# Kernel optimization log

Hardware: AMD Instinct MI355X
Metric: run time of the kernel (lower is better)

Reference implementation:

```python
import jax, jax.numpy as jnp
import numpy as np

B, N = 32, 256
PHI1, PHI2 = 64, 128
RHO1, RHO2, OUT = 256, 128, 64


def setup_inputs() -> dict:
    key = jax.random.key(0)
    ks = jax.random.split(key, 12)
    dm = jax.random.normal(ks[0], (B, N, N), dtype=jnp.float32)
    lengths = jnp.clip(jax.random.randint(ks[1], (B,), 0, N), 2, N).astype(jnp.int32)

    def lin(k, fan_in, fan_out):
        # torch nn.Linear default init: U(-1/sqrt(fan_in), 1/sqrt(fan_in))
        bound = 1.0 / np.sqrt(fan_in)
        kw, kb = jax.random.split(k)
        W = jax.random.uniform(kw, (fan_in, fan_out), jnp.float32, -bound, bound)
        b = jax.random.uniform(kb, (fan_out,), jnp.float32, -bound, bound)
        return W, b

    W1, b1 = lin(ks[2], 1, PHI1)
    W2, b2 = lin(ks[3], PHI1, PHI2)
    W3, b3 = lin(ks[4], PHI2, RHO1)
    W4, b4 = lin(ks[5], RHO1, RHO2)
    W5, b5 = lin(ks[6], RHO2, OUT)
    return {"dm": dm, "lengths": lengths, "W1": W1, "b1": b1, "W2": W2, "b2": b2,
            "W3": W3, "b3": b3, "W4": W4, "b4": b4, "W5": W5, "b5": b5}


def reference(dm, lengths, W1, b1, W2, b2, W3, b3, W4, b4, W5, b5):
    # Static upper-triangular (offset=1) index pairs: P = N*(N-1)/2
    iu0, iu1 = jnp.triu_indices(N, k=1)
    scalars = dm[:, iu0, iu1]                                   # [B, P]
    # Ragged mask: a pair (i, j) exists only if both indices < item length
    mask = (iu0[None, :] < lengths[:, None]) & (iu1[None, :] < lengths[:, None])  # [B, P]
    # phi MLP applied per scalar: 1 -> 64 -> 128, ReLU after each
    h = jax.nn.relu(scalars[..., None] * W1[0] + b1)            # [B, P, 64]
    h = jax.nn.relu(jnp.einsum('bpd,de->bpe', h, W2) + b2)      # [B, P, 128]
    # Masked sum-pool over pairs
    pooled = jnp.sum(h * mask[..., None].astype(h.dtype), axis=1)  # [B, 128]
    # rho MLP: 128 -> 256 -> 128 -> OUT (ReLU on hidden layers only)
    r = jax.nn.relu(pooled @ W3 + b3)
    r = jax.nn.relu(r @ W4 + b4)
    return r @ W5 + b5                                           # [B, OUT]
```

## Files before the change

kernel.cpp:

```cpp
#include <hip/hip_runtime.h>
#include <hip/hip_bf16.h>


#define NB 32
#define NN 256
#define PHI2 128
#define SEGS 65

__global__ __launch_bounds__(128) void build_tables(
    const float* __restrict__ W1, const float* __restrict__ b1,
    const float* __restrict__ W2, const float* __restrict__ b2,
    float4* __restrict__ table4,
    float* __restrict__ tsort, float* __restrict__ pooled) {
  __shared__ float w2_s[64 * PHI2];
  __shared__ float t_s[64], w1_s[64], b1_s[64];
  __shared__ float a_sh[128], b_sh[128];
  __shared__ int cat_s[64], rank_s[64];
  const int tid = threadIdx.x;
  const int seg = blockIdx.x;
  const float4* W2v = (const float4*)W2;
  float4* w2v = (float4*)w2_s;
  for (int i = tid; i < 64 * PHI2 / 4; i += 128) w2v[i] = W2v[i];
  if (tid < 64) {
    float w = W1[tid], bb = b1[tid];
    w1_s[tid] = w; b1_s[tid] = bb;
    int cat; float t;
    if (w > 0.f)      { cat = 0; t = -bb / w; }
    else if (w < 0.f) { cat = 1; t = -bb / w; }
    else              { cat = (bb > 0.f) ? 2 : 3; t = 0.f; }
    t_s[tid] = t; cat_s[tid] = cat;
  }
  __syncthreads();
  if (tid < 64) {
    float t = t_s[tid]; int r = 0;
    for (int k = 0; k < 64; ++k) {
      float tk = t_s[k];
      r += (tk < t) || (tk == t && k < tid);
    }
    rank_s[tid] = r;
    if (seg == 0) tsort[r] = t;
  }
  __syncthreads();
  float a = 0.f, bsum = b2[tid];
#pragma unroll 8
  for (int j = 0; j < 64; ++j) {
    int cat = cat_s[j], r = rank_s[j];
    bool act = (cat == 0) ? (seg > r) : (cat == 1) ? (seg <= r) : (cat == 2);
    float w2 = w2_s[j * PHI2 + tid];
    float m = act ? 1.f : 0.f;
    a    = fmaf(m * w1_s[j], w2, a);
    bsum = fmaf(m * b1_s[j], w2, bsum);
  }
  a_sh[tid] = a; b_sh[tid] = bsum;
  __syncthreads();
  if (tid < 64)
    table4[seg * 64 + tid] =
        make_float4(a_sh[tid], b_sh[tid], a_sh[tid + 64], b_sh[tid + 64]);
  if (seg == 0) {
    for (int i = tid; i < NB * PHI2; i += 128) pooled[i] = 0.f;
  }
}

__device__ __forceinline__ void visit(float comp, int L, float tv, int lane,
                                      const float4* ab_s, float& acc0,
                                      float& acc1) {
  float s = __int_as_float(__builtin_amdgcn_readlane(__float_as_int(comp), L));
  int pos = (int)__popcll(__ballot(tv < s));
  float4 p = ab_s[pos * 64 + lane];
  acc0 += fmaxf(fmaf(p.x, s, p.y), 0.f);
  acc1 += fmaxf(fmaf(p.z, s, p.w), 0.f);
}

__device__ __forceinline__ void visit_dyn(const float4& f4, int j, float tv,
                                          int lane, const float4* ab_s,
                                          float& acc0, float& acc1) {
  int c = j & 3;
  float comp = (c == 0) ? f4.x : (c == 1) ? f4.y : (c == 2) ? f4.z : f4.w;
  visit(comp, j >> 2, tv, lane, ab_s, acc0, acc1);
}

__device__ __forceinline__ void do_row(const float4& f4, int i0, int len,
                                       int half, float tv, int lane,
                                       const float4* ab_s, float& acc0,
                                       float& acc1) {
  const int jlo = i0 + 1, jhi = len - 1;
  const int fullLo = (jlo + 3) >> 2;
  const int fullHi = (jhi >= 3) ? ((jhi - 3) >> 2) : -1;
  if (fullLo > fullHi) {
    for (int j = jlo; j <= jhi; ++j)
      if (((j >> 2) & 1) == half) visit_dyn(f4, j, tv, lane, ab_s, acc0, acc1);
    return;
  }
  for (int j = jlo; j < fullLo * 4; ++j)
    if (((j >> 2) & 1) == half) visit_dyn(f4, j, tv, lane, ab_s, acc0, acc1);
  int L0 = fullLo + (((fullLo & 1) != half) ? 1 : 0);
#pragma unroll 2
  for (int L = L0; L <= fullHi; L += 2) {
    visit(f4.x, L, tv, lane, ab_s, acc0, acc1);
    visit(f4.y, L, tv, lane, ab_s, acc0, acc1);
    visit(f4.z, L, tv, lane, ab_s, acc0, acc1);
    visit(f4.w, L, tv, lane, ab_s, acc0, acc1);
  }
  for (int j = fullHi * 4 + 4; j <= jhi; ++j)
    if (((j >> 2) & 1) == half) visit_dyn(f4, j, tv, lane, ab_s, acc0, acc1);
}

__global__ __launch_bounds__(1024, 8) void phi_pool(
    const float* __restrict__ dm, const int* __restrict__ lengths,
    const float4* __restrict__ table4, const float* __restrict__ tsort,
    float* __restrict__ pooled) {
  __shared__ float4 ab_s[SEGS * 64];
  const int c_row = blockIdx.x >> 1;
  const int half  = blockIdx.x & 1;
  const int b     = blockIdx.y;
  const int tid = threadIdx.x;
  const int lane = tid & 63, w = tid >> 6;

  const int len = lengths[b];
  if (c_row * 16 > len - 2 && 239 - c_row * 16 > len - 2) return;

  for (int i = tid; i < SEGS * 64; i += 1024) ab_s[i] = table4[i];
  __syncthreads();

  const float tv = tsort[lane];
  const float* dmb = dm + (size_t)b * (NN * NN);
  float acc0 = 0.f, acc1 = 0.f;

  const int rA = c_row * 16 + w;
  const int rB = 254 - rA;
  const float4 fA = ((const float4*)(dmb + rA * NN))[lane];
  const float4 fB = ((const float4*)(dmb + rB * NN))[lane];
  if (rA <= len - 2) do_row(fA, rA, len, half, tv, lane, ab_s, acc0, acc1);
  if (rB != rA && rB <= len - 2)
    do_row(fB, rB, len, half, tv, lane, ab_s, acc0, acc1);

  atomicAdd(&pooled[b * PHI2 + lane], acc0);
  atomicAdd(&pooled[b * PHI2 + 64 + lane], acc1);
}

__global__ __launch_bounds__(256) void rho_mlp(
    const float* __restrict__ pooled,
    const float* __restrict__ W3, const float* __restrict__ b3,
    const float* __restrict__ W4, const float* __restrict__ b4,
    const float* __restrict__ W5, const float* __restrict__ b5,
    float* __restrict__ out) {
  __shared__ float w_s[128 * 256];
  __shared__ float p_s[128], r1_s[256], r2_s[128];
  const int b = blockIdx.x, tid = threadIdx.x;
  float4* wsv = (float4*)w_s;
  {
    const float4* w3v = (const float4*)W3;
    for (int i = tid; i < 8192; i += 256) wsv[i] = w3v[i];
  }
  if (tid < 128) p_s[tid] = pooled[b * 128 + tid];
  __syncthreads();
  {
    float acc = b3[tid];
#pragma unroll 8
    for (int k = 0; k < 128; ++k) acc = fmaf(p_s[k], w_s[k * 256 + tid], acc);
    r1_s[tid] = fmaxf(acc, 0.f);
  }
  __syncthreads();
  {
    const float4* w4v = (const float4*)W4;
    for (int i = tid; i < 8192; i += 256) wsv[i] = w4v[i];
  }
  __syncthreads();
  if (tid < 128) {
    float acc = b4[tid];
#pragma unroll 8
    for (int k = 0; k < 256; ++k) acc = fmaf(r1_s[k], w_s[k * 128 + tid], acc);
    r2_s[tid] = fmaxf(acc, 0.f);
  }
  __syncthreads();
  {
    const float4* w5v = (const float4*)W5;
    for (int i = tid; i < 2048; i += 256) wsv[i] = w5v[i];
  }
  __syncthreads();
  if (tid < 64) {
    float acc = b5[tid];
#pragma unroll 8
    for (int k = 0; k < 128; ++k) acc = fmaf(r2_s[k], w_s[k * 64 + tid], acc);
    out[b * 64 + tid] = acc;
  }
}

extern "C" void kernel_launch(void* const* d_in, const int* in_sizes, int n_in,
                              void* d_out, int out_size, void* d_ws, size_t ws_size,
                              hipStream_t stream) {
  const float* dm      = (const float*)d_in[0];
  const int*   lengths = (const int*)d_in[1];
  const float* W1 = (const float*)d_in[2];
  const float* b1 = (const float*)d_in[3];
  const float* W2 = (const float*)d_in[4];
  const float* b2 = (const float*)d_in[5];
  const float* W3 = (const float*)d_in[6];
  const float* b3 = (const float*)d_in[7];
  const float* W4 = (const float*)d_in[8];
  const float* b4 = (const float*)d_in[9];
  const float* W5 = (const float*)d_in[10];
  const float* b5 = (const float*)d_in[11];

  float* ws = (float*)d_ws;
  float4* table4 = (float4*)ws;
  float* tsort   = ws + 16640;
  float* pooled  = ws + 16704;

  build_tables<<<SEGS, 128, 0, stream>>>(W1, b1, W2, b2, table4, tsort, pooled);
  phi_pool<<<dim3(16, NB), 1024, 0, stream>>>(dm, lengths, table4, tsort, pooled);
  rho_mlp<<<NB, 256, 0, stream>>>(pooled, W3, b3, W4, b4, W5, b5, (float*)d_out);
}
```

Baseline: 133.3 us.

## Fuse rho MLP into phi pooling kernel via last-block atomic counter

```diff
diff --git a/kernel.cpp b/kernel.cpp
--- a/kernel.cpp
+++ b/kernel.cpp
@@ -11,7 +11,8 @@
     const float* __restrict__ W1, const float* __restrict__ b1,
     const float* __restrict__ W2, const float* __restrict__ b2,
     float4* __restrict__ table4,
-    float* __restrict__ tsort, float* __restrict__ pooled) {
+    float* __restrict__ tsort, float* __restrict__ pooled,
+    int* __restrict__ ctr) {
   __shared__ float w2_s[64 * PHI2];
   __shared__ float t_s[64], w1_s[64], b1_s[64];
   __shared__ float a_sh[128], b_sh[128];
@@ -58,6 +59,7 @@
         make_float4(a_sh[tid], b_sh[tid], a_sh[tid + 64], b_sh[tid + 64]);
   if (seg == 0) {
     for (int i = tid; i < NB * PHI2; i += 128) pooled[i] = 0.f;
+    if (tid < NB) ctr[tid] = 0;
   }
 }
 
@@ -105,11 +107,17 @@
     if (((j >> 2) & 1) == half) visit_dyn(f4, j, tv, lane, ab_s, acc0, acc1);
 }
 
-__global__ __launch_bounds__(1024, 8) void phi_pool(
+__global__ __launch_bounds__(1024, 8) void phi_pool_rho(
     const float* __restrict__ dm, const int* __restrict__ lengths,
     const float4* __restrict__ table4, const float* __restrict__ tsort,
-    float* __restrict__ pooled) {
+    float* __restrict__ pooled, int* __restrict__ ctr,
+    const float* __restrict__ W3, const float* __restrict__ b3,
+    const float* __restrict__ W4, const float* __restrict__ b4,
+    const float* __restrict__ W5, const float* __restrict__ b5,
+    float* __restrict__ out) {
   __shared__ float4 ab_s[SEGS * 64];
+  __shared__ float p_s[128], r1_s[256], r2_s[128];
+  __shared__ int lastflag;
   const int c_row = blockIdx.x >> 1;
   const int half  = blockIdx.x & 1;
   const int b     = blockIdx.y;
@@ -117,72 +125,90 @@
   const int lane = tid & 63, w = tid >> 6;
 
   const int len = lengths[b];
-  if (c_row * 16 > len - 2 && 239 - c_row * 16 > len - 2) return;
-
-  for (int i = tid; i < SEGS * 64; i += 1024) ab_s[i] = table4[i];
-  __syncthreads();
-
-  const float tv = tsort[lane];
-  const float* dmb = dm + (size_t)b * (NN * NN);
-  float acc0 = 0.f, acc1 = 0.f;
-
-  const int rA = c_row * 16 + w;
-  const int rB = 254 - rA;
-  const float4 fA = ((const float4*)(dmb + rA * NN))[lane];
-  const float4 fB = ((const float4*)(dmb + rB * NN))[lane];
-  if (rA <= len - 2) do_row(fA, rA, len, half, tv, lane, ab_s, acc0, acc1);
-  if (rB != rA && rB <= len - 2)
-    do_row(fB, rB, len, half, tv, lane, ab_s, acc0, acc1);
-
-  atomicAdd(&pooled[b * PHI2 + lane], acc0);
-  atomicAdd(&pooled[b * PHI2 + 64 + lane], acc1);
-}
-
-__global__ __launch_bounds__(256) void rho_mlp(
-    const float* __restrict__ pooled,
-    const float* __restrict__ W3, const float* __restrict__ b3,
-    const float* __restrict__ W4, const float* __restrict__ b4,
-    const float* __restrict__ W5, const float* __restrict__ b5,
-    float* __restrict__ out) {
-  __shared__ float w_s[128 * 256];
-  __shared__ float p_s[128], r1_s[256], r2_s[128];
-  const int b = blockIdx.x, tid = threadIdx.x;
-  float4* wsv = (float4*)w_s;
+  const bool work = !(c_row * 16 > len - 2 && 239 - c_row * 16 > len - 2);
+
+  if (work) {
+    for (int i = tid; i < SEGS * 64; i += 1024) ab_s[i] = table4[i];
+    __syncthreads();
+
+    const float tv = tsort[lane];
+    const float* dmb = dm + (size_t)b * (NN * NN);
+    float acc0 = 0.f, acc1 = 0.f;
+
+    const int rA = c_row * 16 + w;
+    const int rB = 254 - rA;
+    const float4 fA = ((const float4*)(dmb + rA * NN))[lane];
+    const float4 fB = ((const float4*)(dmb + rB * NN))[lane];
+    if (rA <= len - 2) do_row(fA, rA, len, half, tv, lane, ab_s, acc0, acc1);
+    if (rB != rA && rB <= len - 2)
+      do_row(fB, rB, len, half, tv, lane, ab_s, acc0, acc1);
+
+    atomicAdd(&pooled[b * PHI2 + lane], acc0);
+    atomicAdd(&pooled[b * PHI2 + 64 + lane], acc1);
+  }
+
+  __threadfence();
+  if (tid == 0) lastflag = (atomicAdd(&ctr[b], 1) == 15);
+  __syncthreads();
+  if (!lastflag) return;
+
+  if (tid < 128) p_s[tid] = atomicAdd(&pooled[b * PHI2 + tid], 0.0f);
+
+  float* wbuf = (float*)ab_s;
+  float4* wbv = (float4*)wbuf;
+
+  float acc = (tid < 256) ? b3[tid] : 0.f;
   {
     const float4* w3v = (const float4*)W3;
-    for (int i = tid; i < 8192; i += 256) wsv[i] = w3v[i];
-  }
-  if (tid < 128) p_s[tid] = pooled[b * 128 + tid];
-  __syncthreads();
-  {
-    float acc = b3[tid];
-#pragma unroll 8
-    for (int k = 0; k < 128; ++k) acc = fmaf(p_s[k], w_s[k * 256 + tid], acc);
-    r1_s[tid] = fmaxf(acc, 0.f);
-  }
-  __syncthreads();
+    __syncthreads();
+    for (int i = tid; i < 4096; i += 1024) wbv[i] = w3v[i];
+    __syncthreads();
+    if (tid < 256) {
+#pragma unroll 8
+      for (int k = 0; k < 64; ++k) acc = fmaf(p_s[k], wbuf[k * 256 + tid], acc);
+    }
+    __syncthreads();
+    for (int i = tid; i < 4096; i += 1024) wbv[i] = w3v[4096 + i];
+    __syncthreads();
+    if (tid < 256) {
+#pragma unroll 8
+      for (int k = 0; k < 64; ++k)
+        acc = fmaf(p_s[64 + k], wbuf[k * 256 + tid], acc);
+      r1_s[tid] = fmaxf(acc, 0.f);
+    }
+  }
   {
     const float4* w4v = (const float4*)W4;
-    for (int i = tid; i < 8192; i += 256) wsv[i] = w4v[i];
-  }
-  __syncthreads();
-  if (tid < 128) {
-    float acc = b4[tid];
-#pragma unroll 8
-    for (int k = 0; k < 256; ++k) acc = fmaf(r1_s[k], w_s[k * 128 + tid], acc);
-    r2_s[tid] = fmaxf(acc, 0.f);
-  }
-  __syncthreads();
+    __syncthreads();
+    for (int i = tid; i < 4096; i += 1024) wbv[i] = w4v[i];
+    __syncthreads();
+    float a2 = (tid < 128) ? b4[tid] : 0.f;
+    if (tid < 128) {
+#pragma unroll 8
+      for (int k = 0; k < 128; ++k)
+        a2 = fmaf(r1_s[k], wbuf[k * 128 + tid], a2);
+    }
+    __syncthreads();
+    for (int i = tid; i < 4096; i += 1024) wbv[i] = w4v[4096 + i];
+    __syncthreads();
+    if (tid < 128) {
+#pragma unroll 8
+      for (int k = 0; k < 128; ++k)
+        a2 = fmaf(r1_s[128 + k], wbuf[k * 128 + tid], a2);
+      r2_s[tid] = fmaxf(a2, 0.f);
+    }
+  }
   {
     const float4* w5v = (const float4*)W5;
-    for (int i = tid; i < 2048; i += 256) wsv[i] = w5v[i];
-  }
-  __syncthreads();
-  if (tid < 64) {
-    float acc = b5[tid];
-#pragma unroll 8
-    for (int k = 0; k < 128; ++k) acc = fmaf(r2_s[k], w_s[k * 64 + tid], acc);
-    out[b * 64 + tid] = acc;
+    __syncthreads();
+    for (int i = tid; i < 2048; i += 1024) wbv[i] = w5v[i];
+    __syncthreads();
+    if (tid < 64) {
+      float a3 = b5[tid];
+#pragma unroll 8
+      for (int k = 0; k < 128; ++k) a3 = fmaf(r2_s[k], wbuf[k * 64 + tid], a3);
+      out[b * 64 + tid] = a3;
+    }
   }
 }
 
@@ -206,8 +232,11 @@
   float4* table4 = (float4*)ws;
   float* tsort   = ws + 16640;
   float* pooled  = ws + 16704;
-
-  build_tables<<<SEGS, 128, 0, stream>>>(W1, b1, W2, b2, table4, tsort, pooled);
-  phi_pool<<<dim3(16, NB), 1024, 0, stream>>>(dm, lengths, table4, tsort, pooled);
-  rho_mlp<<<NB, 256, 0, stream>>>(pooled, W3, b3, W4, b4, W5, b5, (float*)d_out);
-}
+  int*   ctr     = (int*)(ws + 20800);
+
+  build_tables<<<SEGS, 128, 0, stream>>>(W1, b1, W2, b2, table4, tsort,
+                                         pooled, ctr);
+  phi_pool_rho<<<dim3(16, NB), 1024, 0, stream>>>(
+      dm, lengths, table4, tsort, pooled, ctr,
+      W3, b3, W4, b4, W5, b5, (float*)d_out);
+}
```

Result: slower. 245.0 us (+83.9%).
